# Kernel optimization log

Hardware: AMD Instinct MI355X
Metric: run time of the kernel (lower is better)

The kernel has to match this reference:

```python
import jax, jax.numpy as jnp
import numpy as np

N_QUBITS = 11
N_CIRCUITS = 3
N_ROTS = 6
BATCH = 512
C64 = jnp.complex64


def _ry_mat(theta):
    # RY(t) = [[cos t/2, -sin t/2], [sin t/2, cos t/2]]
    c = jnp.cos(theta * 0.5)
    s = jnp.sin(theta * 0.5)
    return jnp.stack([jnp.stack([c, -s]), jnp.stack([s, c])]).astype(C64)


def _rz_mat(theta):
    # RZ(t) = diag(e^{-i t/2}, e^{+i t/2})
    e = jnp.exp((-0.5j) * theta.astype(C64))
    z = jnp.zeros_like(e)
    return jnp.stack([jnp.stack([e, z]), jnp.stack([z, jnp.conj(e)])])


def _apply_1q(state, U, q):
    # state: (2,)*n complex; apply 2x2 U on axis q (PennyLane wire q = axis q)
    out = jnp.tensordot(U, state, axes=((1,), (q,)))
    return jnp.moveaxis(out, 0, q)


def _apply_ctrl(state, U, c, t):
    # controlled-U on wires [c(control), t(target)]: block_diag(I2, U) in |c t> basis
    U4 = jnp.eye(4, dtype=C64).at[2:, 2:].set(U)
    out = jnp.tensordot(U4.reshape(2, 2, 2, 2), state, axes=((2, 3), (c, t)))
    return jnp.moveaxis(out, (0, 1), (c, t))


def _simulate(angles):
    # angles: [n_circuits, 6, n_qubits] -> expvals [2*n_qubits] (X then Z)
    n = N_QUBITS
    state = jnp.zeros((2,) * n, dtype=C64).at[(0,) * n].set(1.0)
    for i in range(N_CIRCUITS):
        for q in range(n):
            state = _apply_1q(state, _ry_mat(angles[i, 0, q]), q)
            state = _apply_1q(state, _rz_mat(angles[i, 1, q]), q)
            state = _apply_1q(state, _ry_mat(angles[i, 2, q]), q)
            state = _apply_1q(state, _rz_mat(angles[i, 3, q]), q)
        for q in range(n):
            t = (q + 1) % n
            state = _apply_ctrl(state, _ry_mat(angles[i, 4, q]), q, t)
            state = _apply_ctrl(state, _rz_mat(angles[i, 5, q]), q, t)
    ex_x, ex_z = [], []
    for q in range(n):
        s0 = jnp.take(state, 0, axis=q)
        s1 = jnp.take(state, 1, axis=q)
        # <X_q> = 2 Re <psi_{q=0}|psi_{q=1}>,  <Z_q> = p(q=0) - p(q=1)
        ex_x.append(2.0 * jnp.real(jnp.vdot(s0, s1)))
        ex_z.append(jnp.sum(jnp.abs(s0) ** 2 - jnp.abs(s1) ** 2))
    return jnp.stack(ex_x + ex_z).astype(jnp.float32)


def setup_inputs() -> dict:
    key = jax.random.key(0)
    k1, k2, k3 = jax.random.split(key, 3)
    x = jax.random.normal(k1, (BATCH, N_QUBITS), dtype=jnp.float32)
    W = jax.random.uniform(k2, (N_CIRCUITS, N_QUBITS * N_ROTS, N_QUBITS),
                           dtype=jnp.float32, minval=-0.01, maxval=0.01)
    b = jax.random.uniform(k3, (N_CIRCUITS, N_QUBITS * N_ROTS),
                           dtype=jnp.float32, minval=-0.01, maxval=0.01)
    return {"x": x, "W": W, "b": b}


def reference(x, W, b):
    # per-circuit Linear (dropout is identity in eval): [B, C, n_rots*n_qubits]
    rot = jnp.einsum('coi,bi->bco', W, x) + b[None, :, :]
    angles = rot.reshape(x.shape[0], N_CIRCUITS, N_ROTS, N_QUBITS)
    return jax.vmap(_simulate)(angles)  # [B, 2*n_qubits]
```

## Files before the change

kernel.cpp:

```cpp
#include <hip/hip_runtime.h>

#define NQ 11
#define NC 3
#define NANG (NC * 66)
#define BLOCK 256

typedef float f2 __attribute__((ext_vector_type(2)));

__device__ __forceinline__ f2 swp(f2 v) { return __builtin_shufflevector(v, v, 1, 0); }

template<int CTRL>
__device__ __forceinline__ float dppx(float v) {
  return __int_as_float(__builtin_amdgcn_update_dpp(
      0, __float_as_int(v), CTRL, 0xF, 0xF, false));
}
template<int CTRL>
__device__ __forceinline__ f2 dpp2(f2 v) {
  f2 r; r.x = dppx<CTRL>(v.x); r.y = dppx<CTRL>(v.y); return r;
}
template<int OFF>
__device__ __forceinline__ float swz1(float v) {
  return __int_as_float(__builtin_amdgcn_ds_swizzle(__float_as_int(v), OFF));
}
template<int OFF>
__device__ __forceinline__ f2 swz2(f2 v) {
  f2 r; r.x = swz1<OFF>(v.x); r.y = swz1<OFF>(v.y); return r;
}
__device__ __forceinline__ float plp16(float v, int lane) {
  auto r = __builtin_amdgcn_permlane16_swap(__float_as_int(v), __float_as_int(v), false, false);
  return __int_as_float((lane & 16) ? r[0] : r[1]);
}
__device__ __forceinline__ float plp32(float v, int lane) {
  auto r = __builtin_amdgcn_permlane32_swap(__float_as_int(v), __float_as_int(v), false, false);
  return __int_as_float((lane & 32) ? r[0] : r[1]);
}
__device__ __forceinline__ f2 plp16_2(f2 v, int lane) {
  f2 r; r.x = plp16(v.x, lane); r.y = plp16(v.y, lane); return r;
}
__device__ __forceinline__ f2 plp32_2(f2 v, int lane) {
  f2 r; r.x = plp32(v.x, lane); r.y = plp32(v.y, lane); return r;
}
__device__ __forceinline__ float plsum16(float v) {
  auto r = __builtin_amdgcn_permlane16_swap(__float_as_int(v), __float_as_int(v), false, false);
  return __int_as_float(r[0]) + __int_as_float(r[1]);
}
__device__ __forceinline__ float plsum32(float v) {
  auto r = __builtin_amdgcn_permlane32_swap(__float_as_int(v), __float_as_int(v), false, false);
  return __int_as_float(r[0]) + __int_as_float(r[1]);
}

__device__ __forceinline__ void apply2p(f2& v0, f2& v1, float4 U) {
  const f2 ai2 = {-U.y, U.y};
  const f2 bi2 = {-U.w, U.w};
  const f2 w0 = swp(v0), w1 = swp(v1);
  const f2 n0 =  U.x * v0 + ai2 * w0 + U.z * v1 + bi2 * w1;
  const f2 n1 = -U.z * v0 + bi2 * w0 + U.x * v1 - ai2 * w1;
  v0 = n0; v1 = n1;
}
__device__ __forceinline__ void gpartp(f2& v, f2 p, float4 U, bool hi) {
  const f2 ai2 = hi ? f2{U.y, -U.y} : f2{-U.y, U.y};
  const float br = hi ? -U.z : U.z;
  const f2 bi2 = {-U.w, U.w};
  v = U.x * v + ai2 * swp(v) + br * p + bi2 * swp(p);
}
__device__ __forceinline__ float4 su2mul(float4 A, float4 B) {
  return make_float4(
    (A.x*B.x - A.y*B.y) - (A.z*B.z + A.w*B.w),
    (A.x*B.y + A.y*B.x) - (A.w*B.z - A.z*B.w),
    (A.x*B.z - A.y*B.w) + (A.z*B.x + A.w*B.y),
    (A.x*B.w + A.y*B.z) + (A.w*B.x - A.z*B.y));
}
template<int WVX>
__device__ __forceinline__ void g_wave8(f2 (&s)[8], float4 U, f2* buf, int wave, int lane) {
  const int base = (wave << 6) | lane;
#pragma unroll
  for (int i = 0; i < 8; ++i) buf[(i << 8) | base] = s[i];
  __syncthreads();
  const int pbase = ((wave ^ WVX) << 6) | lane;
  const bool hi = (wave & WVX) != 0;
#pragma unroll
  for (int i = 0; i < 8; ++i) gpartp(s[i], buf[(i << 8) | pbase], U, hi);
}

__global__ __launch_bounds__(BLOCK) void qsim_kernel(
    const float* __restrict__ x, const float* __restrict__ W,
    const float* __restrict__ bias, float* __restrict__ out) {
  const int bidx = blockIdx.x;
  const int tid = threadIdx.x;
  const int lane = tid & 63, wave = tid >> 6;

  __shared__ float xs[NQ];
  __shared__ float ang[NANG];
  __shared__ float4 m1s[NC * NQ];
  __shared__ float4 m2s[NC * NQ];
  __shared__ float4 v1s[NC * 10];
  __shared__ float4 js[2];
  __shared__ f2 ex0[2048];
  __shared__ f2 ex1[2048];
  __shared__ float red[4][24];

  if (tid < NQ) xs[tid] = x[bidx * NQ + tid];
  __syncthreads();

  if (tid < NANG) {
    const int c = tid / 66, o = tid - c * 66;
    const float* wr = W + (c * 66 + o) * NQ;
    float s = bias[c * 66 + o];
#pragma unroll
    for (int i = 0; i < NQ; ++i) s += wr[i] * xs[i];
    ang[tid] = s;
  }
  __syncthreads();

  if (tid < 2 * NC * NQ) {
    const int kind = tid / (NC * NQ);
    const int id = tid - kind * (NC * NQ);
    const int c = id / NQ, q = id - c * NQ;
    const float* a = ang + c * 66;
    if (kind == 0) {
      float s0,c0,s1,c1,s2,c2,s3,c3;
      sincosf(0.5f*a[q],      &s0,&c0);
      sincosf(0.5f*a[11+q],   &s1,&c1);
      sincosf(0.5f*a[22+q],   &s2,&c2);
      sincosf(0.5f*a[33+q],   &s3,&c3);
      const float mar = c1*c0, mai = -s1*c0;
      const float mbr = -c1*s0, mbi = s1*s0;
      const float nar = c2*mar + s2*mbr, nai = c2*mai - s2*mbi;
      const float nbr = c2*mbr - s2*mar, nbi = c2*mbi + s2*mai;
      m1s[id] = make_float4(c3*nar + s3*nai, c3*nai - s3*nar,
                            c3*nbr + s3*nbi, c3*nbi - s3*nbr);
    } else {
      float s4,c4,s5,c5;
      sincosf(0.5f*a[44+q], &s4,&c4);
      sincosf(0.5f*a[55+q], &s5,&c5);
      m2s[id] = make_float4(c5*c4, -s5*c4, -c5*s4, s5*s4);
    }
  }
  __syncthreads();

  if (tid < NC * 10) {
    const int c = tid / 10, tt = tid - c * 10, t = tt + 1;
    v1s[tid] = su2mul(m2s[c*NQ + t - 1], m1s[c*NQ + t]);
  } else if (tid < NC * 10 + 2) {
    const int cc = tid - NC * 10;
    js[cc] = su2mul(m1s[(cc + 1) * NQ], m2s[cc * NQ + 10]);
  }
  __syncthreads();

  f2 s[8];
#pragma unroll
  for (int i = 0; i < 8; ++i) s[i] = f2{0.f, 0.f};
  if (tid == 0) s[0].x = 1.f;

  for (int c = 0; c < NC; ++c) {
    const float4* M1 = &m1s[c * NQ];
    const float4* VF = &v1s[c * 10];
    if (c == 0) {
      const float4 U = M1[0];
#pragma unroll
      for (int r = 0; r < 8; r += 2) apply2p(s[r], s[r + 1], U);
    }
    {
      const bool hi = (lane & 32) != 0;
#pragma unroll
      for (int r = 0; r < 8; ++r)
        gpartp(s[r], plp32_2(s[r], lane), (r & 1) ? VF[0] : M1[1], hi);
    }
    {
      const float4 U = *((lane & 32) ? &VF[1] : &M1[2]);
      const bool hi = (lane & 16) != 0;
#pragma unroll
      for (int r = 0; r < 8; ++r) gpartp(s[r], plp16_2(s[r], lane), U, hi);
    }
    {
      const float4 U = *((lane & 16) ? &VF[2] : &M1[3]);
      const bool hi = (lane & 8) != 0;
#pragma unroll
      for (int r = 0; r < 8; ++r) gpartp(s[r], swz2<0x201F>(s[r]), U, hi);
    }
    {
      const float4 U = *((lane & 8) ? &VF[3] : &M1[4]);
      const bool hi = (lane & 4) != 0;
#pragma unroll
      for (int r = 0; r < 8; ++r) gpartp(s[r], swz2<0x101F>(s[r]), U, hi);
    }
    g_wave8<2>(s, *((lane & 4) ? &VF[4] : &M1[5]), ex0, wave, lane);
    g_wave8<1>(s, *((wave & 2) ? &VF[5] : &M1[6]), ex1, wave, lane);
    {
      const float4 U = *((wave & 1) ? &VF[6] : &M1[7]);
      const bool hi = (lane & 2) != 0;
#pragma unroll
      for (int r = 0; r < 8; ++r) gpartp(s[r], dpp2<0x4E>(s[r]), U, hi);
    }
    {
      const float4 U = *((lane & 2) ? &VF[7] : &M1[8]);
      const bool hi = (lane & 1) != 0;
#pragma unroll
      for (int r = 0; r < 8; ++r) gpartp(s[r], dpp2<0xB1>(s[r]), U, hi);
    }
    {
      const float4 U = *((lane & 1) ? &VF[8] : &M1[9]);
      apply2p(s[0], s[2], U); apply2p(s[1], s[3], U);
      apply2p(s[4], s[6], U); apply2p(s[5], s[7], U);
    }
    {
      const float4 U0 = M1[10], U1 = VF[9];
      apply2p(s[0], s[4], U0); apply2p(s[1], s[5], U0);
      apply2p(s[2], s[6], U1); apply2p(s[3], s[7], U1);
    }
    if (c < 2) {
      const float4 Un = m1s[(c + 1) * NQ];
      const float4 Uj = js[c];
      apply2p(s[0], s[1], Un); apply2p(s[2], s[3], Un);
      apply2p(s[4], s[5], Uj); apply2p(s[6], s[7], Uj);
    } else {
      const float4 U = m2s[c * NQ + 10];
      apply2p(s[4], s[5], U); apply2p(s[6], s[7], U);
    }
  }

  const int base = (wave << 6) | lane;
#pragma unroll
  for (int i = 0; i < 8; ++i) ex0[(i << 8) | base] = s[i];
  __syncthreads();
  const int pb2 = ((wave ^ 2) << 6) | lane;
  const int pb1 = ((wave ^ 1) << 6) | lane;
  f2 aq5 = {0,0}, aq6 = {0,0};
#pragma unroll
  for (int i = 0; i < 8; ++i) {
    aq5 += s[i] * ex0[(i << 8) | pb2];
    aq6 += s[i] * ex0[(i << 8) | pb1];
  }
  f2 zt = {0,0}, z0v = {0,0}, z9v = {0,0}, z10v = {0,0};
#pragma unroll
  for (int r = 0; r < 8; ++r) {
    const f2 m = s[r] * s[r];
    zt += m;
    z0v  += (r & 1) ? -m : m;
    z9v  += (r & 2) ? -m : m;
    z10v += (r & 4) ? -m : m;
  }
  f2 aq0 = {0,0}, aq9 = {0,0}, aq10 = {0,0};
#pragma unroll
  for (int r = 0; r < 8; ++r) {
    aq0  += s[r] * s[r ^ 1];
    aq9  += s[r] * s[r ^ 2];
    aq10 += s[r] * s[r ^ 4];
  }
  f2 aq1={0,0}, aq2={0,0}, aq3={0,0}, aq4={0,0}, aq7={0,0}, aq8={0,0};
#pragma unroll
  for (int r = 0; r < 8; ++r) {
    aq1 += s[r] * plp32_2(s[r], lane);
    aq2 += s[r] * plp16_2(s[r], lane);
    aq3 += s[r] * swz2<0x201F>(s[r]);
    aq4 += s[r] * swz2<0x101F>(s[r]);
    aq7 += s[r] * dpp2<0x4E>(s[r]);
    aq8 += s[r] * dpp2<0xB1>(s[r]);
  }
  const float ztot = zt.x + zt.y;

  float v[22];
  v[0]=aq0.x+aq0.y; v[1]=aq1.x+aq1.y; v[2]=aq2.x+aq2.y; v[3]=aq3.x+aq3.y;
  v[4]=aq4.x+aq4.y; v[5]=aq5.x+aq5.y; v[6]=aq6.x+aq6.y;
  v[7]=aq7.x+aq7.y; v[8]=aq8.x+aq8.y; v[9]=aq9.x+aq9.y; v[10]=aq10.x+aq10.y;
  v[11] = z0v.x + z0v.y;
  v[12] = (lane & 32) ? -ztot : ztot;
  v[13] = (lane & 16) ? -ztot : ztot;
  v[14] = (lane & 8)  ? -ztot : ztot;
  v[15] = (lane & 4)  ? -ztot : ztot;
  v[16] = (wave & 2)  ? -ztot : ztot;
  v[17] = (wave & 1)  ? -ztot : ztot;
  v[18] = (lane & 2)  ? -ztot : ztot;
  v[19] = (lane & 1)  ? -ztot : ztot;
  v[20] = z9v.x + z9v.y;
  v[21] = z10v.x + z10v.y;

#pragma unroll
  for (int k = 0; k < 22; ++k) {
    v[k] += dppx<0xB1>(v[k]);
    v[k] += dppx<0x4E>(v[k]);
  }
  const int q4l = lane & 3;
  float wv[6];
#pragma unroll
  for (int p = 0; p < 5; ++p)
    wv[p] = q4l == 0 ? v[4*p] : (q4l == 1 ? v[4*p+1] : (q4l == 2 ? v[4*p+2] : v[4*p+3]));
  wv[5] = q4l == 0 ? v[20] : (q4l == 1 ? v[21] : 0.f);
#pragma unroll
  for (int p = 0; p < 6; ++p) {
    wv[p] += swz1<0x101F>(wv[p]);
    wv[p] += swz1<0x201F>(wv[p]);
    wv[p] = plsum16(wv[p]);
    wv[p] = plsum32(wv[p]);
  }
  if (lane < 4) {
#pragma unroll
    for (int p = 0; p < 6; ++p) red[wave][4*p + lane] = wv[p];
  }
  __syncthreads();
  if (tid < 22) {
    float sacc = 0.f;
#pragma unroll
    for (int w4 = 0; w4 < 4; ++w4) sacc += red[w4][tid];
    out[bidx * 22 + tid] = sacc;
  }
}

extern "C" void kernel_launch(void* const* d_in, const int* in_sizes, int n_in,
                              void* d_out, int out_size, void* d_ws, size_t ws_size,
                              hipStream_t stream) {
  (void)n_in; (void)d_ws; (void)ws_size; (void)out_size;
  const float* x = (const float*)d_in[0];
  const float* W = (const float*)d_in[1];
  const float* b = (const float*)d_in[2];
  float* out = (float*)d_out;
  const int batch = in_sizes[0] / NQ;
  qsim_kernel<<<batch, BLOCK, 0, stream>>>(x, W, b, out);
}
```

Baseline: 20.26 us.

## Use 128-thread blocks with 16 amplitudes per thread and one LDS exchange

The state-vector simulation now runs on 2 waves instead of 4, so each thread holds 16 amplitudes and three qubits live in registers rather than two. This needs only one cross-wave LDS exchange per circuit instead of two, which removes a barrier round, and that exchange uses float4 stores. The exchange buffers alternate between circuits, and the final <X> term for the cross-wave qubit uses a single LDS round. The cost is higher register pressure and half as many threads per block, so each block has less parallelism to hide latency.

```diff
diff --git a/kernel.cpp b/kernel.cpp
--- a/kernel.cpp
+++ b/kernel.cpp
@@ -3,7 +3,7 @@
 #define NQ 11
 #define NC 3
 #define NANG (NC * 66)
-#define BLOCK 256
+#define BLOCK 128
 
 typedef float f2 __attribute__((ext_vector_type(2)));
 
@@ -70,16 +70,20 @@
     (A.x*B.z - A.y*B.w) + (A.z*B.x + A.w*B.y),
     (A.x*B.w + A.y*B.z) + (A.w*B.x - A.z*B.y));
 }
-template<int WVX>
-__device__ __forceinline__ void g_wave8(f2 (&s)[8], float4 U, f2* buf, int wave, int lane) {
+__device__ __forceinline__ void g_wave16(f2 (&s)[16], float4 U, float4* buf, int wave, int lane) {
   const int base = (wave << 6) | lane;
 #pragma unroll
-  for (int i = 0; i < 8; ++i) buf[(i << 8) | base] = s[i];
-  __syncthreads();
-  const int pbase = ((wave ^ WVX) << 6) | lane;
-  const bool hi = (wave & WVX) != 0;
-#pragma unroll
-  for (int i = 0; i < 8; ++i) gpartp(s[i], buf[(i << 8) | pbase], U, hi);
+  for (int i = 0; i < 8; ++i)
+    buf[(i << 7) | base] = make_float4(s[2*i].x, s[2*i].y, s[2*i+1].x, s[2*i+1].y);
+  __syncthreads();
+  const int pbase = ((wave ^ 1) << 6) | lane;
+  const bool hi = (wave & 1) != 0;
+#pragma unroll
+  for (int i = 0; i < 8; ++i) {
+    const float4 p = buf[(i << 7) | pbase];
+    gpartp(s[2*i],   f2{p.x, p.y}, U, hi);
+    gpartp(s[2*i+1], f2{p.z, p.w}, U, hi);
+  }
 }
 
 __global__ __launch_bounds__(BLOCK) void qsim_kernel(
@@ -95,20 +99,24 @@
   __shared__ float4 m2s[NC * NQ];
   __shared__ float4 v1s[NC * 10];
   __shared__ float4 js[2];
-  __shared__ f2 ex0[2048];
-  __shared__ f2 ex1[2048];
-  __shared__ float red[4][24];
+  __shared__ float4 ex0[1024];
+  __shared__ float4 ex1[1024];
+  __shared__ float red[2][24];
 
   if (tid < NQ) xs[tid] = x[bidx * NQ + tid];
   __syncthreads();
 
-  if (tid < NANG) {
-    const int c = tid / 66, o = tid - c * 66;
-    const float* wr = W + (c * 66 + o) * NQ;
-    float s = bias[c * 66 + o];
-#pragma unroll
-    for (int i = 0; i < NQ; ++i) s += wr[i] * xs[i];
-    ang[tid] = s;
+#pragma unroll
+  for (int r2 = 0; r2 < 2; ++r2) {
+    const int id = tid + 128 * r2;
+    if (id < NANG) {
+      const int c = id / 66, o = id - c * 66;
+      const float* wr = W + (c * 66 + o) * NQ;
+      float s = bias[c * 66 + o];
+#pragma unroll
+      for (int i = 0; i < NQ; ++i) s += wr[i] * xs[i];
+      ang[id] = s;
+    }
   }
   __syncthreads();
 
@@ -147,9 +155,9 @@
   }
   __syncthreads();
 
-  f2 s[8];
-#pragma unroll
-  for (int i = 0; i < 8; ++i) s[i] = f2{0.f, 0.f};
+  f2 s[16];
+#pragma unroll
+  for (int i = 0; i < 16; ++i) s[i] = f2{0.f, 0.f};
   if (tid == 0) s[0].x = 1.f;
 
   for (int c = 0; c < NC; ++c) {
@@ -158,104 +166,119 @@
     if (c == 0) {
       const float4 U = M1[0];
 #pragma unroll
-      for (int r = 0; r < 8; r += 2) apply2p(s[r], s[r + 1], U);
+      for (int r = 0; r < 16; r += 2) apply2p(s[r], s[r + 1], U);
     }
     {
       const bool hi = (lane & 32) != 0;
-#pragma unroll
-      for (int r = 0; r < 8; ++r)
-        gpartp(s[r], plp32_2(s[r], lane), (r & 1) ? VF[0] : M1[1], hi);
+      const float4 U0 = M1[1], U1 = VF[0];
+#pragma unroll
+      for (int r = 0; r < 16; ++r)
+        gpartp(s[r], plp32_2(s[r], lane), (r & 1) ? U1 : U0, hi);
     }
     {
       const float4 U = *((lane & 32) ? &VF[1] : &M1[2]);
       const bool hi = (lane & 16) != 0;
 #pragma unroll
-      for (int r = 0; r < 8; ++r) gpartp(s[r], plp16_2(s[r], lane), U, hi);
+      for (int r = 0; r < 16; ++r) gpartp(s[r], plp16_2(s[r], lane), U, hi);
     }
     {
       const float4 U = *((lane & 16) ? &VF[2] : &M1[3]);
       const bool hi = (lane & 8) != 0;
 #pragma unroll
-      for (int r = 0; r < 8; ++r) gpartp(s[r], swz2<0x201F>(s[r]), U, hi);
-    }
-    {
-      const float4 U = *((lane & 8) ? &VF[3] : &M1[4]);
+      for (int r = 0; r < 16; ++r) gpartp(s[r], swz2<0x201F>(s[r]), U, hi);
+    }
+    g_wave16(s, *((lane & 8) ? &VF[3] : &M1[4]), (c & 1) ? ex1 : ex0, wave, lane);
+    {
+      const float4 U = *((wave & 1) ? &VF[4] : &M1[5]);
       const bool hi = (lane & 4) != 0;
 #pragma unroll
-      for (int r = 0; r < 8; ++r) gpartp(s[r], swz2<0x101F>(s[r]), U, hi);
-    }
-    g_wave8<2>(s, *((lane & 4) ? &VF[4] : &M1[5]), ex0, wave, lane);
-    g_wave8<1>(s, *((wave & 2) ? &VF[5] : &M1[6]), ex1, wave, lane);
-    {
-      const float4 U = *((wave & 1) ? &VF[6] : &M1[7]);
+      for (int r = 0; r < 16; ++r) gpartp(s[r], swz2<0x101F>(s[r]), U, hi);
+    }
+    {
+      const float4 U = *((lane & 4) ? &VF[5] : &M1[6]);
       const bool hi = (lane & 2) != 0;
 #pragma unroll
-      for (int r = 0; r < 8; ++r) gpartp(s[r], dpp2<0x4E>(s[r]), U, hi);
-    }
-    {
-      const float4 U = *((lane & 2) ? &VF[7] : &M1[8]);
+      for (int r = 0; r < 16; ++r) gpartp(s[r], dpp2<0x4E>(s[r]), U, hi);
+    }
+    {
+      const float4 U = *((lane & 2) ? &VF[6] : &M1[7]);
       const bool hi = (lane & 1) != 0;
 #pragma unroll
-      for (int r = 0; r < 8; ++r) gpartp(s[r], dpp2<0xB1>(s[r]), U, hi);
-    }
-    {
-      const float4 U = *((lane & 1) ? &VF[8] : &M1[9]);
-      apply2p(s[0], s[2], U); apply2p(s[1], s[3], U);
-      apply2p(s[4], s[6], U); apply2p(s[5], s[7], U);
+      for (int r = 0; r < 16; ++r) gpartp(s[r], dpp2<0xB1>(s[r]), U, hi);
+    }
+    {
+      const float4 U = *((lane & 1) ? &VF[7] : &M1[8]);
+      apply2p(s[0], s[2], U);  apply2p(s[1], s[3], U);
+      apply2p(s[4], s[6], U);  apply2p(s[5], s[7], U);
+      apply2p(s[8], s[10], U); apply2p(s[9], s[11], U);
+      apply2p(s[12], s[14], U); apply2p(s[13], s[15], U);
+    }
+    {
+      const float4 U0 = M1[9], U1 = VF[8];
+      apply2p(s[0], s[4], U0);  apply2p(s[1], s[5], U0);
+      apply2p(s[2], s[6], U1);  apply2p(s[3], s[7], U1);
+      apply2p(s[8], s[12], U0); apply2p(s[9], s[13], U0);
+      apply2p(s[10], s[14], U1); apply2p(s[11], s[15], U1);
     }
     {
       const float4 U0 = M1[10], U1 = VF[9];
-      apply2p(s[0], s[4], U0); apply2p(s[1], s[5], U0);
-      apply2p(s[2], s[6], U1); apply2p(s[3], s[7], U1);
+      apply2p(s[0], s[8], U0);  apply2p(s[1], s[9], U0);
+      apply2p(s[2], s[10], U0); apply2p(s[3], s[11], U0);
+      apply2p(s[4], s[12], U1); apply2p(s[5], s[13], U1);
+      apply2p(s[6], s[14], U1); apply2p(s[7], s[15], U1);
     }
     if (c < 2) {
       const float4 Un = m1s[(c + 1) * NQ];
       const float4 Uj = js[c];
-      apply2p(s[0], s[1], Un); apply2p(s[2], s[3], Un);
-      apply2p(s[4], s[5], Uj); apply2p(s[6], s[7], Uj);
+#pragma unroll
+      for (int r = 0; r < 16; r += 2) apply2p(s[r], s[r + 1], (r & 8) ? Uj : Un);
     } else {
       const float4 U = m2s[c * NQ + 10];
-      apply2p(s[4], s[5], U); apply2p(s[6], s[7], U);
+#pragma unroll
+      for (int r = 8; r < 16; r += 2) apply2p(s[r], s[r + 1], U);
     }
   }
 
   const int base = (wave << 6) | lane;
 #pragma unroll
-  for (int i = 0; i < 8; ++i) ex0[(i << 8) | base] = s[i];
-  __syncthreads();
-  const int pb2 = ((wave ^ 2) << 6) | lane;
-  const int pb1 = ((wave ^ 1) << 6) | lane;
-  f2 aq5 = {0,0}, aq6 = {0,0};
+  for (int i = 0; i < 8; ++i)
+    ex1[(i << 7) | base] = make_float4(s[2*i].x, s[2*i].y, s[2*i+1].x, s[2*i+1].y);
+  __syncthreads();
+  const int pbase = ((wave ^ 1) << 6) | lane;
+  f2 aq4 = {0,0};
 #pragma unroll
   for (int i = 0; i < 8; ++i) {
-    aq5 += s[i] * ex0[(i << 8) | pb2];
-    aq6 += s[i] * ex0[(i << 8) | pb1];
-  }
-  f2 zt = {0,0}, z0v = {0,0}, z9v = {0,0}, z10v = {0,0};
-#pragma unroll
-  for (int r = 0; r < 8; ++r) {
+    const float4 p = ex1[(i << 7) | pbase];
+    aq4 += s[2*i] * f2{p.x, p.y} + s[2*i+1] * f2{p.z, p.w};
+  }
+
+  f2 zt = {0,0}, z0v = {0,0}, z8v = {0,0}, z9v = {0,0}, z10v = {0,0};
+#pragma unroll
+  for (int r = 0; r < 16; ++r) {
     const f2 m = s[r] * s[r];
     zt += m;
     z0v  += (r & 1) ? -m : m;
-    z9v  += (r & 2) ? -m : m;
-    z10v += (r & 4) ? -m : m;
-  }
-  f2 aq0 = {0,0}, aq9 = {0,0}, aq10 = {0,0};
-#pragma unroll
-  for (int r = 0; r < 8; ++r) {
+    z8v  += (r & 2) ? -m : m;
+    z9v  += (r & 4) ? -m : m;
+    z10v += (r & 8) ? -m : m;
+  }
+  f2 aq0 = {0,0}, aq8 = {0,0}, aq9 = {0,0}, aq10 = {0,0};
+#pragma unroll
+  for (int r = 0; r < 16; ++r) {
     aq0  += s[r] * s[r ^ 1];
-    aq9  += s[r] * s[r ^ 2];
-    aq10 += s[r] * s[r ^ 4];
-  }
-  f2 aq1={0,0}, aq2={0,0}, aq3={0,0}, aq4={0,0}, aq7={0,0}, aq8={0,0};
-#pragma unroll
-  for (int r = 0; r < 8; ++r) {
+    aq8  += s[r] * s[r ^ 2];
+    aq9  += s[r] * s[r ^ 4];
+    aq10 += s[r] * s[r ^ 8];
+  }
+  f2 aq1={0,0}, aq2={0,0}, aq3={0,0}, aq5={0,0}, aq6={0,0}, aq7={0,0};
+#pragma unroll
+  for (int r = 0; r < 16; ++r) {
     aq1 += s[r] * plp32_2(s[r], lane);
     aq2 += s[r] * plp16_2(s[r], lane);
     aq3 += s[r] * swz2<0x201F>(s[r]);
-    aq4 += s[r] * swz2<0x101F>(s[r]);
-    aq7 += s[r] * dpp2<0x4E>(s[r]);
-    aq8 += s[r] * dpp2<0xB1>(s[r]);
+    aq5 += s[r] * swz2<0x101F>(s[r]);
+    aq6 += s[r] * dpp2<0x4E>(s[r]);
+    aq7 += s[r] * dpp2<0xB1>(s[r]);
   }
   const float ztot = zt.x + zt.y;
 
@@ -267,11 +290,11 @@
   v[12] = (lane & 32) ? -ztot : ztot;
   v[13] = (lane & 16) ? -ztot : ztot;
   v[14] = (lane & 8)  ? -ztot : ztot;
-  v[15] = (lane & 4)  ? -ztot : ztot;
-  v[16] = (wave & 2)  ? -ztot : ztot;
-  v[17] = (wave & 1)  ? -ztot : ztot;
-  v[18] = (lane & 2)  ? -ztot : ztot;
-  v[19] = (lane & 1)  ? -ztot : ztot;
+  v[15] = (wave & 1)  ? -ztot : ztot;
+  v[16] = (lane & 4)  ? -ztot : ztot;
+  v[17] = (lane & 2)  ? -ztot : ztot;
+  v[18] = (lane & 1)  ? -ztot : ztot;
+  v[19] = z8v.x + z8v.y;
   v[20] = z9v.x + z9v.y;
   v[21] = z10v.x + z10v.y;
 
@@ -299,10 +322,7 @@
   }
   __syncthreads();
   if (tid < 22) {
-    float sacc = 0.f;
-#pragma unroll
-    for (int w4 = 0; w4 < 4; ++w4) sacc += red[w4][tid];
-    out[bidx * 22 + tid] = sacc;
+    out[bidx * 22 + tid] = red[0][tid] + red[1][tid];
   }
 }
 
```

Measured after the change: 27.84 us. 37.4% more time.
